# Performance work log

Measured on AMD Instinct MI355X. Metric: run time of the kernel, lower is better.

Reference implementation:

```python
import jax, jax.numpy as jnp
import numpy as np

B, N_QUBITS, N_LAYERS = 128, 14, 4


def _rx(theta):
    c = jnp.cos(theta / 2).astype(jnp.complex64)
    s = (-1j) * jnp.sin(theta / 2).astype(jnp.complex64)
    return jnp.stack([jnp.stack([c, s], -1), jnp.stack([s, c], -1)], -2)


def _ry(theta):
    c = jnp.cos(theta / 2)
    s = jnp.sin(theta / 2)
    return jnp.stack([jnp.stack([c, -s], -1), jnp.stack([s, c], -1)], -2).astype(jnp.complex64)


def _rz(theta):
    p = jnp.exp((-0.5j) * theta.astype(jnp.complex64))
    q = jnp.exp((0.5j) * theta.astype(jnp.complex64))
    z = jnp.zeros_like(p)
    return jnp.stack([jnp.stack([p, z], -1), jnp.stack([z, q], -1)], -2)


def _apply_1q(state, U, wire):
    # state: (B, 2, 2, ..., 2); U: (2,2) shared or (B,2,2) per-sample
    s = jnp.moveaxis(state, wire + 1, 1)
    if U.ndim == 2:
        s = jnp.einsum('ij,bj...->bi...', U, s)
    else:
        s = jnp.einsum('bij,bj...->bi...', U, s)
    return jnp.moveaxis(s, 1, wire + 1)


def _cnot(state, c, t):
    s = jnp.moveaxis(state, (c + 1, t + 1), (1, 2))  # (B, 2c, 2t, rest)
    s = jnp.concatenate([s[:, :1], s[:, 1:, ::-1]], axis=1)  # flip target where control=1
    return jnp.moveaxis(s, (1, 2), (c + 1, t + 1))


def _layer(state, rx_l, ry_l, rz_l, ent_l, n):
    for i in range(n):
        state = _apply_1q(state, _rx(rx_l[i]), i)
        state = _apply_1q(state, _ry(ry_l[i]), i)
        state = _apply_1q(state, _rz(rz_l[i]), i)
    for i in range(n - 1):
        state = _cnot(state, i, i + 1)
        state = _apply_1q(state, _rz(ent_l[i]), i + 1)
    return state


def _circuit(x, rx_p, ry_p, rz_p, ent_p):
    b, n = x.shape
    n_layers = rx_p.shape[0]
    scaled = jnp.tanh(x) * np.pi  # angle encoding, matches torch.tanh(x)*pi
    state = jnp.zeros((b,) + (2,) * n, jnp.complex64)
    state = state.at[(slice(None),) + (0,) * n].set(1.0)  # |0...0> per sample
    for i in range(n):  # per-sample RY encoding
        state = _apply_1q(state, _ry(scaled[:, i]), i)
    for l in range(n_layers):
        state = _layer(state, rx_p[l], ry_p[l], rz_p[l], ent_p[l], n)
    probs = state.real ** 2 + state.imag ** 2  # (B, 2, ..., 2) real
    outs = []
    for i in range(n):  # <Z_i> = P(bit_i=0) - P(bit_i=1)
        p = jnp.moveaxis(probs, i + 1, 1).reshape(b, 2, -1).sum(-1)
        outs.append(p[:, 0] - p[:, 1])
    return jnp.stack(outs, -1)  # (B, n_qubits)


def setup_inputs() -> dict:
    key = jax.random.key(0)
    k1, k2, k3, k4, k5 = jax.random.split(key, 5)
    return {
        'x': jax.random.normal(k1, (B, N_QUBITS), jnp.float32),
        'params_rx': jax.random.normal(k2, (N_LAYERS, N_QUBITS), jnp.float32),
        'params_ry': jax.random.normal(k3, (N_LAYERS, N_QUBITS), jnp.float32),
        'params_rz': jax.random.normal(k4, (N_LAYERS, N_QUBITS), jnp.float32),
        'params_entangle': jax.random.normal(k5, (N_LAYERS, N_QUBITS - 1), jnp.float32),
    }


def reference(x, params_rx, params_ry, params_rz, params_entangle):
    return _circuit(x, params_rx, params_ry, params_rz, params_entangle)
```

## Files before the change

kernel.cpp:

```cpp
#include <hip/hip_runtime.h>
#include <math.h>

#define NQ 14
#define NL 4
#define NS (1 << NQ)
#define NT 1024
#define APT (NS / NT)

struct c32 { float x, y; };
__device__ __forceinline__ c32 cmul(c32 a, c32 b) { return {a.x*b.x - a.y*b.y, a.x*b.y + a.y*b.x}; }
__device__ __forceinline__ c32 cadd(c32 a, c32 b) { return {a.x + b.x, a.y + b.y}; }

__device__ __forceinline__ void gate16(c32* v, const float* U, const int s) {
    float4 u0 = *(const float4*)U;
    float4 u1 = *(const float4*)(U + 4);
    c32 a00={u0.x,u0.y}, a01={u0.z,u0.w}, a10={u1.x,u1.y}, a11={u1.z,u1.w};
    #pragma unroll
    for (int k = 0; k < 16; ++k) {
        if (k & s) continue;
        c32 A = v[k], B = v[k | s];
        v[k]     = cadd(cmul(a00, A), cmul(a01, B));
        v[k | s] = cadd(cmul(a10, A), cmul(a11, B));
    }
}

__device__ __forceinline__ void gate8(c32* v, const float* U, const int s) {
    float4 u0 = *(const float4*)U;
    float4 u1 = *(const float4*)(U + 4);
    c32 a00={u0.x,u0.y}, a01={u0.z,u0.w}, a10={u1.x,u1.y}, a11={u1.z,u1.w};
    #pragma unroll
    for (int k = 0; k < 8; ++k) {
        if (k & s) continue;
        c32 A = v[k], B = v[k | s];
        v[k]     = cadd(cmul(a00, A), cmul(a01, B));
        v[k | s] = cadd(cmul(a10, A), cmul(a11, B));
    }
}

__device__ __forceinline__ void gate8sw(c32* v, const float* U, const int s, const int sw) {
    float4 u0 = *(const float4*)U;
    float4 u1 = *(const float4*)(U + 4);
    c32 n00={u0.x,u0.y}, n01={u0.z,u0.w}, n10={u1.x,u1.y}, n11={u1.z,u1.w};
    c32 a00 = sw ? n11 : n00;
    c32 a01 = sw ? n10 : n01;
    c32 a10 = sw ? n01 : n10;
    c32 a11 = sw ? n00 : n11;
    #pragma unroll
    for (int k = 0; k < 8; ++k) {
        if (k & s) continue;
        c32 A = v[k], B = v[k | s];
        v[k]     = cadd(cmul(a00, A), cmul(a01, B));
        v[k | s] = cadd(cmul(a10, A), cmul(a11, B));
    }
}

__device__ __forceinline__ void precompute(const float* x, const float* prx, const float* pry,
                                           const float* prz, const float* pent,
                                           float (*Um)[NQ][8], float (*tlo)[128], float (*thi)[64],
                                           float* encc, float* encs, int tid, int samp) {
    if (tid < NL*NQ) {
        int l = tid / NQ, q = tid % NQ;
        float hx = 0.5f*prx[l*NQ+q], hy = 0.5f*pry[l*NQ+q], hz = 0.5f*prz[l*NQ+q];
        float cx = cosf(hx), sx = sinf(hx);
        float cy = cosf(hy), sy = sinf(hy);
        float cz = cosf(hz), sz = sinf(hz);
        c32 m00 = { cy*cx,  sy*sx };
        c32 m01 = {-sy*cx, -cy*sx };
        c32 m10 = { sy*cx, -cy*sx };
        c32 m11 = { cy*cx, -sy*sx };
        c32 e0 = {cz, -sz}, e1 = {cz, sz};
        c32 u00 = cmul(e0, m00), u01 = cmul(e0, m01);
        c32 u10 = cmul(e1, m10), u11 = cmul(e1, m11);
        float* U = Um[l][q];
        U[0]=u00.x; U[1]=u00.y; U[2]=u01.x; U[3]=u01.y;
        U[4]=u10.x; U[5]=u10.y; U[6]=u11.x; U[7]=u11.y;
    } else if (tid >= 64 && tid < 64 + NL*192) {
        int t2 = tid - 64;
        int l = t2 / 192, r = t2 % 192;
        if (r < 128) {
            float a = 0.f;
            for (int p = 0; p < 7; ++p) {
                float th = 0.5f * pent[l*(NQ-1) + (12 - p)];
                a += ((r >> p) & 1) ? th : -th;
            }
            tlo[l][r] = a;
        } else {
            int m = r - 128;
            float a = 0.f;
            for (int p = 0; p < 6; ++p) {
                float th = 0.5f * pent[l*(NQ-1) + (5 - p)];
                a += ((m >> p) & 1) ? th : -th;
            }
            thi[l][m] = a;
        }
    } else if (tid >= 960 && tid < 960 + NQ) {
        int i = tid - 960;
        float th = tanhf(x[samp*NQ + i]) * 3.14159265358979323846f;
        encc[i] = cosf(0.5f*th);
        encs[i] = sinf(0.5f*th);
    }
}

__device__ __forceinline__ void passP2(float2* st, const float (*UmL)[8], int tid) {
    const int ib = ((tid >> 6) << 10) | (tid & 63);
    c32 v[16];
    #pragma unroll
    for (int k = 0; k < 16; ++k) { float2 f = st[ib + k*64]; v[k] = {f.x, f.y}; }
    gate16(v, UmL[4], 8);
    gate16(v, UmL[5], 4);
    gate16(v, UmL[6], 2);
    gate16(v, UmL[7], 1);
    #pragma unroll
    for (int k = 0; k < 16; ++k) st[ib + k*64] = make_float2(v[k].x, v[k].y);
}

__device__ __forceinline__ void passP3(float2* st, const float (*UmL)[8], int tid) {
    #pragma unroll 1
    for (int m = 0; m < 2; ++m) {
        const int T  = tid + m*NT;
        const int ib = ((T >> 3) << 6) | (T & 7);
        c32 v[8];
        #pragma unroll
        for (int k = 0; k < 8; ++k) { float2 f = st[ib + k*8]; v[k] = {f.x, f.y}; }
        gate8(v, UmL[8], 4);
        gate8(v, UmL[9], 2);
        gate8(v, UmL[10], 1);
        #pragma unroll
        for (int k = 0; k < 8; ++k) st[ib + k*8] = make_float2(v[k].x, v[k].y);
    }
}

__device__ __forceinline__ void passP4(float2* st, const float (*UmL)[8], int tid) {
    const int t4   = tid & 15;
    const int base = tid << 4;
    #pragma unroll 1
    for (int m = 0; m < 2; ++m) {
        c32 v[8];
        #pragma unroll
        for (int s = 0; s < 8; ++s) {
            float2 f = st[base | (((m << 3) | s) ^ t4)];
            v[s] = {f.x, f.y};
        }
        gate8sw(v, UmL[11], 4, (t4 >> 2) & 1);
        gate8sw(v, UmL[12], 2, (t4 >> 1) & 1);
        gate8sw(v, UmL[13], 1,  t4       & 1);
        #pragma unroll
        for (int s = 0; s < 8; ++s)
            st[base | (((m << 3) | s) ^ t4)] = make_float2(v[s].x, v[s].y);
    }
}

__global__ __launch_bounds__(NT) __attribute__((amdgpu_waves_per_eu(4, 4)))
void qc_kernel(const float* __restrict__ x,
               const float* __restrict__ prx,
               const float* __restrict__ pry,
               const float* __restrict__ prz,
               const float* __restrict__ pent,
               float* __restrict__ out)
{
    __shared__ float2 st[NS];
    __shared__ float  Um[NL][NQ][8];
    __shared__ float  tlo[NL][128];
    __shared__ float  thi[NL][64];
    __shared__ float  encc[NQ], encs[NQ];
    __shared__ float  red[NT/64][NQ];

    const int tid = threadIdx.x;
    const int b   = blockIdx.x;

    precompute(x, prx, pry, prz, pent, Um, tlo, thi, encc, encs, tid, b);
    __syncthreads();

    {
        float prodLow = 1.f;
        #pragma unroll
        for (int p = 0; p < 10; ++p)
            prodLow *= ((tid >> p) & 1) ? encs[13-p] : encc[13-p];
        c32 v[16];
        #pragma unroll
        for (int j = 0; j < 16; ++j) {
            float a = prodLow
                    * ((j & 8) ? encs[0] : encc[0])
                    * ((j & 4) ? encs[1] : encc[1])
                    * ((j & 2) ? encs[2] : encc[2])
                    * ((j & 1) ? encs[3] : encc[3]);
            v[j] = { a, 0.f };
        }
        gate16(v, Um[0][0], 8);
        gate16(v, Um[0][1], 4);
        gate16(v, Um[0][2], 2);
        gate16(v, Um[0][3], 1);
        #pragma unroll
        for (int j = 0; j < 16; ++j) st[tid + j*NT] = make_float2(v[j].x, v[j].y);
    }
    __syncthreads();
    passP2(st, Um[0], tid); __syncthreads();
    passP3(st, Um[0], tid); __syncthreads();
    passP4(st, Um[0], tid); __syncthreads();

    #pragma unroll 1
    for (int l = 1; l < NL; ++l) {
        {
            const float* phlo = tlo[l-1];
            const float* phhi = thi[l-1];
            c32 v[16];
            #pragma unroll
            for (int j = 0; j < 16; ++j) {
                int y  = tid + j*NT;
                int a  = y ^ (y >> 1);
                float2 f = st[a];
                float ang = phlo[y & 127] + phhi[(y >> 7) & 63];
                float sn, cs;
                __sincosf(ang, &sn, &cs);
                v[j] = { cs*f.x - sn*f.y, cs*f.y + sn*f.x };
            }
            __syncthreads();
            gate16(v, Um[l][0], 8);
            gate16(v, Um[l][1], 4);
            gate16(v, Um[l][2], 2);
            gate16(v, Um[l][3], 1);
            #pragma unroll
            for (int j = 0; j < 16; ++j) st[tid + j*NT] = make_float2(v[j].x, v[j].y);
        }
        __syncthreads();
        passP2(st, Um[l], tid); __syncthreads();
        passP3(st, Um[l], tid); __syncthreads();
        passP4(st, Um[l], tid); __syncthreads();
    }

    float acc[NQ];
    #pragma unroll
    for (int i = 0; i < NQ; ++i) acc[i] = 0.f;
    #pragma unroll
    for (int j = 0; j < APT; ++j) {
        int y = tid + j*NT;
        int a = y ^ (y >> 1);
        float2 f = st[a];
        float ang = tlo[NL-1][y & 127] + thi[NL-1][(y >> 7) & 63];
        float sn, cs;
        __sincosf(ang, &sn, &cs);
        float re = cs*f.x - sn*f.y;
        float im = cs*f.y + sn*f.x;
        float pr = re*re + im*im;
        #pragma unroll
        for (int p = 0; p < NQ; ++p)
            acc[NQ-1-p] += ((y >> p) & 1) ? -pr : pr;
    }
    #pragma unroll
    for (int off = 32; off >= 1; off >>= 1) {
        #pragma unroll
        for (int i = 0; i < NQ; ++i)
            acc[i] += __shfl_down(acc[i], off, 64);
    }
    const int wid = tid >> 6, lane = tid & 63;
    if (lane == 0) {
        #pragma unroll
        for (int i = 0; i < NQ; ++i) red[wid][i] = acc[i];
    }
    __syncthreads();
    if (tid < NQ) {
        float s = 0.f;
        #pragma unroll
        for (int w = 0; w < NT/64; ++w) s += red[w][tid];
        out[b*NQ + tid] = s;
    }
}

extern "C" void kernel_launch(void* const* d_in, const int* in_sizes, int n_in,
                              void* d_out, int out_size, void* d_ws, size_t ws_size,
                              hipStream_t stream) {
    (void)d_ws; (void)ws_size; (void)n_in; (void)out_size;
    const float* x    = (const float*)d_in[0];
    const float* prx  = (const float*)d_in[1];
    const float* pry  = (const float*)d_in[2];
    const float* prz  = (const float*)d_in[3];
    const float* pent = (const float*)d_in[4];
    float* out = (float*)d_out;
    const int B = in_sizes[0] / NQ;
    qc_kernel<<<B, NT, 0, stream>>>(x, prx, pry, prz, pent, out);
}
```

Baseline: 141.9 us.

## Shrink per-thread state to 8 amplitudes and precompute phase tables as cos/sin

Restructures each layer's gate schedule so every pass holds 8 or 4 amplitudes per thread instead of 16. Qubit 0 now moves into a pass with qubits 4-5 using strided addressing, and the later passes are regrouped as 6-8, 9-10 and 11-13. The entangling phase tables now store cos/sin pairs, so per-element sincos becomes a complex multiply. The aim is to cut register pressure at the fixed 4 waves/EU and drop transcendental work, at the cost of an extra pass and barrier per layer and more shared-memory traffic.

```diff
diff --git a/kernel.cpp b/kernel.cpp
--- a/kernel.cpp
+++ b/kernel.cpp
@@ -11,12 +11,17 @@
 __device__ __forceinline__ c32 cmul(c32 a, c32 b) { return {a.x*b.x - a.y*b.y, a.x*b.y + a.y*b.x}; }
 __device__ __forceinline__ c32 cadd(c32 a, c32 b) { return {a.x + b.x, a.y + b.y}; }
 
-__device__ __forceinline__ void gate16(c32* v, const float* U, const int s) {
+__device__ __forceinline__ c32 phase_mul(float2 p1, float2 p2, float2 f) {
+    c32 ph = { p1.x*p2.x - p1.y*p2.y, p1.x*p2.y + p1.y*p2.x };
+    return { ph.x*f.x - ph.y*f.y, ph.x*f.y + ph.y*f.x };
+}
+
+__device__ __forceinline__ void gate8(c32* v, const float* U, const int s) {
     float4 u0 = *(const float4*)U;
     float4 u1 = *(const float4*)(U + 4);
     c32 a00={u0.x,u0.y}, a01={u0.z,u0.w}, a10={u1.x,u1.y}, a11={u1.z,u1.w};
     #pragma unroll
-    for (int k = 0; k < 16; ++k) {
+    for (int k = 0; k < 8; ++k) {
         if (k & s) continue;
         c32 A = v[k], B = v[k | s];
         v[k]     = cadd(cmul(a00, A), cmul(a01, B));
@@ -24,12 +29,12 @@
     }
 }
 
-__device__ __forceinline__ void gate8(c32* v, const float* U, const int s) {
+__device__ __forceinline__ void gate4(c32* v, const float* U, const int s) {
     float4 u0 = *(const float4*)U;
     float4 u1 = *(const float4*)(U + 4);
     c32 a00={u0.x,u0.y}, a01={u0.z,u0.w}, a10={u1.x,u1.y}, a11={u1.z,u1.w};
     #pragma unroll
-    for (int k = 0; k < 8; ++k) {
+    for (int k = 0; k < 4; ++k) {
         if (k & s) continue;
         c32 A = v[k], B = v[k | s];
         v[k]     = cadd(cmul(a00, A), cmul(a01, B));
@@ -54,10 +59,24 @@
     }
 }
 
-__device__ __forceinline__ void precompute(const float* x, const float* prx, const float* pry,
-                                           const float* prz, const float* pent,
-                                           float (*Um)[NQ][8], float (*tlo)[128], float (*thi)[64],
-                                           float* encc, float* encs, int tid, int samp) {
+__global__ __launch_bounds__(NT) __attribute__((amdgpu_waves_per_eu(4, 4)))
+void qc_kernel(const float* __restrict__ x,
+               const float* __restrict__ prx,
+               const float* __restrict__ pry,
+               const float* __restrict__ prz,
+               const float* __restrict__ pent,
+               float* __restrict__ out)
+{
+    __shared__ float2 st[NS];
+    __shared__ float  Um[NL][NQ][8];
+    __shared__ float2 tloc[NL][128];
+    __shared__ float2 thic[NL][64];
+    __shared__ float  encc[NQ], encs[NQ];
+    __shared__ float  red[NT/64][NQ];
+
+    const int tid = threadIdx.x;
+    const int b   = blockIdx.x;
+
     if (tid < NL*NQ) {
         int l = tid / NQ, q = tid % NQ;
         float hx = 0.5f*prx[l*NQ+q], hy = 0.5f*pry[l*NQ+q], hz = 0.5f*prz[l*NQ+q];
@@ -83,7 +102,7 @@
                 float th = 0.5f * pent[l*(NQ-1) + (12 - p)];
                 a += ((r >> p) & 1) ? th : -th;
             }
-            tlo[l][r] = a;
+            tloc[l][r] = make_float2(cosf(a), sinf(a));
         } else {
             int m = r - 128;
             float a = 0.f;
@@ -91,141 +110,138 @@
                 float th = 0.5f * pent[l*(NQ-1) + (5 - p)];
                 a += ((m >> p) & 1) ? th : -th;
             }
-            thi[l][m] = a;
+            thic[l][m] = make_float2(cosf(a), sinf(a));
         }
     } else if (tid >= 960 && tid < 960 + NQ) {
         int i = tid - 960;
-        float th = tanhf(x[samp*NQ + i]) * 3.14159265358979323846f;
+        float th = tanhf(x[b*NQ + i]) * 3.14159265358979323846f;
         encc[i] = cosf(0.5f*th);
         encs[i] = sinf(0.5f*th);
     }
-}
-
-__device__ __forceinline__ void passP2(float2* st, const float (*UmL)[8], int tid) {
-    const int ib = ((tid >> 6) << 10) | (tid & 63);
-    c32 v[16];
-    #pragma unroll
-    for (int k = 0; k < 16; ++k) { float2 f = st[ib + k*64]; v[k] = {f.x, f.y}; }
-    gate16(v, UmL[4], 8);
-    gate16(v, UmL[5], 4);
-    gate16(v, UmL[6], 2);
-    gate16(v, UmL[7], 1);
-    #pragma unroll
-    for (int k = 0; k < 16; ++k) st[ib + k*64] = make_float2(v[k].x, v[k].y);
-}
-
-__device__ __forceinline__ void passP3(float2* st, const float (*UmL)[8], int tid) {
+    __syncthreads();
+
+    {
+        float prodT = 1.f;
+        #pragma unroll
+        for (int p = 0; p < 10; ++p)
+            prodT *= ((tid >> p) & 1) ? encs[13-p] : encc[13-p];
+        #pragma unroll 1
+        for (int h = 0; h < 2; ++h) {
+            float ah = prodT * (h ? encs[0] : encc[0]);
+            c32 v[8];
+            #pragma unroll
+            for (int m = 0; m < 8; ++m) {
+                float a = ah
+                        * ((m & 4) ? encs[1] : encc[1])
+                        * ((m & 2) ? encs[2] : encc[2])
+                        * ((m & 1) ? encs[3] : encc[3]);
+                v[m] = { a, 0.f };
+            }
+            gate8(v, Um[0][1], 4);
+            gate8(v, Um[0][2], 2);
+            gate8(v, Um[0][3], 1);
+            const int yb = (h << 13) | tid;
+            #pragma unroll
+            for (int m = 0; m < 8; ++m) st[yb + (m << 10)] = make_float2(v[m].x, v[m].y);
+        }
+    }
+    __syncthreads();
+
     #pragma unroll 1
-    for (int m = 0; m < 2; ++m) {
-        const int T  = tid + m*NT;
-        const int ib = ((T >> 3) << 6) | (T & 7);
-        c32 v[8];
-        #pragma unroll
-        for (int k = 0; k < 8; ++k) { float2 f = st[ib + k*8]; v[k] = {f.x, f.y}; }
-        gate8(v, UmL[8], 4);
-        gate8(v, UmL[9], 2);
-        gate8(v, UmL[10], 1);
-        #pragma unroll
-        for (int k = 0; k < 8; ++k) st[ib + k*8] = make_float2(v[k].x, v[k].y);
-    }
-}
-
-__device__ __forceinline__ void passP4(float2* st, const float (*UmL)[8], int tid) {
-    const int t4   = tid & 15;
-    const int base = tid << 4;
-    #pragma unroll 1
-    for (int m = 0; m < 2; ++m) {
-        c32 v[8];
-        #pragma unroll
-        for (int s = 0; s < 8; ++s) {
-            float2 f = st[base | (((m << 3) | s) ^ t4)];
-            v[s] = {f.x, f.y};
-        }
-        gate8sw(v, UmL[11], 4, (t4 >> 2) & 1);
-        gate8sw(v, UmL[12], 2, (t4 >> 1) & 1);
-        gate8sw(v, UmL[13], 1,  t4       & 1);
-        #pragma unroll
-        for (int s = 0; s < 8; ++s)
-            st[base | (((m << 3) | s) ^ t4)] = make_float2(v[s].x, v[s].y);
-    }
-}
-
-__global__ __launch_bounds__(NT) __attribute__((amdgpu_waves_per_eu(4, 4)))
-void qc_kernel(const float* __restrict__ x,
-               const float* __restrict__ prx,
-               const float* __restrict__ pry,
-               const float* __restrict__ prz,
-               const float* __restrict__ pent,
-               float* __restrict__ out)
-{
-    __shared__ float2 st[NS];
-    __shared__ float  Um[NL][NQ][8];
-    __shared__ float  tlo[NL][128];
-    __shared__ float  thi[NL][64];
-    __shared__ float  encc[NQ], encs[NQ];
-    __shared__ float  red[NT/64][NQ];
-
-    const int tid = threadIdx.x;
-    const int b   = blockIdx.x;
-
-    precompute(x, prx, pry, prz, pent, Um, tlo, thi, encc, encs, tid, b);
-    __syncthreads();
-
-    {
-        float prodLow = 1.f;
-        #pragma unroll
-        for (int p = 0; p < 10; ++p)
-            prodLow *= ((tid >> p) & 1) ? encs[13-p] : encc[13-p];
-        c32 v[16];
-        #pragma unroll
-        for (int j = 0; j < 16; ++j) {
-            float a = prodLow
-                    * ((j & 8) ? encs[0] : encc[0])
-                    * ((j & 4) ? encs[1] : encc[1])
-                    * ((j & 2) ? encs[2] : encc[2])
-                    * ((j & 1) ? encs[3] : encc[3]);
-            v[j] = { a, 0.f };
-        }
-        gate16(v, Um[0][0], 8);
-        gate16(v, Um[0][1], 4);
-        gate16(v, Um[0][2], 2);
-        gate16(v, Um[0][3], 1);
-        #pragma unroll
-        for (int j = 0; j < 16; ++j) st[tid + j*NT] = make_float2(v[j].x, v[j].y);
-    }
-    __syncthreads();
-    passP2(st, Um[0], tid); __syncthreads();
-    passP3(st, Um[0], tid); __syncthreads();
-    passP4(st, Um[0], tid); __syncthreads();
-
-    #pragma unroll 1
-    for (int l = 1; l < NL; ++l) {
+    for (int l = 0; l < NL; ++l) {
+        if (l > 0) {
+            #pragma unroll 1
+            for (int h = 0; h < 2; ++h) {
+                const int yb = (h << 13) | tid;
+                c32 v[8];
+                #pragma unroll
+                for (int m = 0; m < 8; ++m) {
+                    int y = yb + (m << 10);
+                    int a = y ^ (y >> 1);
+                    float2 f = st[a];
+                    v[m] = phase_mul(tloc[l-1][y & 127], thic[l-1][(y >> 7) & 63], f);
+                }
+                gate8(v, Um[l][1], 4);
+                gate8(v, Um[l][2], 2);
+                gate8(v, Um[l][3], 1);
+                __syncthreads();
+                #pragma unroll
+                for (int m = 0; m < 8; ++m) st[yb + (m << 10)] = make_float2(v[m].x, v[m].y);
+            }
+            __syncthreads();
+        }
+
+        #pragma unroll 1
+        for (int m = 0; m < 2; ++m) {
+            const int T  = tid + (m << 10);
+            const int ib = ((T >> 8) << 10) | (T & 255);
+            c32 v[8];
+            #pragma unroll
+            for (int k = 0; k < 8; ++k) {
+                int a = ib + ((k & 4) ? 8192 : 0) + ((k & 2) ? 512 : 0) + ((k & 1) ? 256 : 0);
+                float2 f = st[a];
+                v[k] = {f.x, f.y};
+            }
+            gate8(v, Um[l][0], 4);
+            gate8(v, Um[l][4], 2);
+            gate8(v, Um[l][5], 1);
+            #pragma unroll
+            for (int k = 0; k < 8; ++k) {
+                int a = ib + ((k & 4) ? 8192 : 0) + ((k & 2) ? 512 : 0) + ((k & 1) ? 256 : 0);
+                st[a] = make_float2(v[k].x, v[k].y);
+            }
+        }
+        __syncthreads();
+
+        #pragma unroll 1
+        for (int m = 0; m < 2; ++m) {
+            const int T  = tid + (m << 10);
+            const int ib = ((T >> 5) << 8) | (T & 31);
+            c32 v[8];
+            #pragma unroll
+            for (int k = 0; k < 8; ++k) { float2 f = st[ib + (k << 5)]; v[k] = {f.x, f.y}; }
+            gate8(v, Um[l][6], 4);
+            gate8(v, Um[l][7], 2);
+            gate8(v, Um[l][8], 1);
+            #pragma unroll
+            for (int k = 0; k < 8; ++k) st[ib + (k << 5)] = make_float2(v[k].x, v[k].y);
+        }
+        __syncthreads();
+
+        #pragma unroll 1
+        for (int m = 0; m < 4; ++m) {
+            const int T  = tid + (m << 10);
+            const int ib = ((T >> 3) << 5) | (T & 7);
+            c32 v[4];
+            #pragma unroll
+            for (int k = 0; k < 4; ++k) { float2 f = st[ib + (k << 3)]; v[k] = {f.x, f.y}; }
+            gate4(v, Um[l][9], 2);
+            gate4(v, Um[l][10], 1);
+            #pragma unroll
+            for (int k = 0; k < 4; ++k) st[ib + (k << 3)] = make_float2(v[k].x, v[k].y);
+        }
+        __syncthreads();
+
         {
-            const float* phlo = tlo[l-1];
-            const float* phhi = thi[l-1];
-            c32 v[16];
-            #pragma unroll
-            for (int j = 0; j < 16; ++j) {
-                int y  = tid + j*NT;
-                int a  = y ^ (y >> 1);
-                float2 f = st[a];
-                float ang = phlo[y & 127] + phhi[(y >> 7) & 63];
-                float sn, cs;
-                __sincosf(ang, &sn, &cs);
-                v[j] = { cs*f.x - sn*f.y, cs*f.y + sn*f.x };
-            }
-            __syncthreads();
-            gate16(v, Um[l][0], 8);
-            gate16(v, Um[l][1], 4);
-            gate16(v, Um[l][2], 2);
-            gate16(v, Um[l][3], 1);
-            #pragma unroll
-            for (int j = 0; j < 16; ++j) st[tid + j*NT] = make_float2(v[j].x, v[j].y);
-        }
-        __syncthreads();
-        passP2(st, Um[l], tid); __syncthreads();
-        passP3(st, Um[l], tid); __syncthreads();
-        passP4(st, Um[l], tid); __syncthreads();
+            const int t4   = tid & 15;
+            const int base = tid << 4;
+            #pragma unroll 1
+            for (int m = 0; m < 2; ++m) {
+                c32 v[8];
+                #pragma unroll
+                for (int s = 0; s < 8; ++s) {
+                    float2 f = st[base | (((m << 3) | s) ^ t4)];
+                    v[s] = {f.x, f.y};
+                }
+                gate8sw(v, Um[l][11], 4, (t4 >> 2) & 1);
+                gate8sw(v, Um[l][12], 2, (t4 >> 1) & 1);
+                gate8sw(v, Um[l][13], 1,  t4       & 1);
+                #pragma unroll
+                for (int s = 0; s < 8; ++s)
+                    st[base | (((m << 3) | s) ^ t4)] = make_float2(v[s].x, v[s].y);
+            }
+        }
+        __syncthreads();
     }
 
     float acc[NQ];
@@ -236,12 +252,8 @@
         int y = tid + j*NT;
         int a = y ^ (y >> 1);
         float2 f = st[a];
-        float ang = tlo[NL-1][y & 127] + thi[NL-1][(y >> 7) & 63];
-        float sn, cs;
-        __sincosf(ang, &sn, &cs);
-        float re = cs*f.x - sn*f.y;
-        float im = cs*f.y + sn*f.x;
-        float pr = re*re + im*im;
+        c32 r = phase_mul(tloc[NL-1][y & 127], thic[NL-1][(y >> 7) & 63], f);
+        float pr = r.x*r.x + r.y*r.y;
         #pragma unroll
         for (int p = 0; p < NQ; ++p)
             acc[NQ-1-p] += ((y >> p) & 1) ? -pr : pr;
```

Measured after the change: 132.6 us. -6.6%, faster.
